# Kernel tuning notes

Measured on AMD Instinct MI355X. Metric: run time of the kernel, lower is better.

The kernel has to match this reference:

```python
import jax, jax.numpy as jnp
import numpy as np

B, DIM, T = 8, 1024, 4096
CB, CD = 4096, 8          # codebook_size, codebook_dim
COMMIT = 0.25
EPS = 1e-12


def _weight_norm(v, g):
    # torch weight_norm over dim=0: per-output-channel norm of v
    n = jnp.sqrt(jnp.sum(v * v, axis=1, keepdims=True))
    return g[:, None] * v / n


def _l2_normalize(x):
    n = jnp.sqrt(jnp.sum(x * x, axis=1, keepdims=True))
    return x / jnp.maximum(n, EPS)


def setup_inputs() -> dict:
    key = jax.random.key(0)
    ks = jax.random.split(key, 5)
    z = jax.random.normal(ks[0], (B, DIM, T), jnp.float32)
    v_in = jax.random.normal(ks[1], (CD, DIM), jnp.float32) * 0.02   # conv1d k=1 weight (squeezed)
    g_in = jnp.sqrt(jnp.sum(v_in * v_in, axis=1))                     # weight_norm init: g = ||v||
    b_in = jnp.zeros((CD,), jnp.float32)
    codebook = jax.random.normal(ks[2], (CB, CD), jnp.float32)        # nn.Embedding default N(0,1)
    v_out = jax.random.normal(ks[3], (DIM, CD), jnp.float32) * 0.02
    g_out = jnp.sqrt(jnp.sum(v_out * v_out, axis=1))
    b_out = jnp.zeros((DIM,), jnp.float32)
    return {"z": z, "v_in": v_in, "g_in": g_in, "b_in": b_in,
            "codebook": codebook, "v_out": v_out, "g_out": g_out, "b_out": b_out}


def reference(z, v_in, g_in, b_in, codebook, v_out, g_out, b_out):
    # in_proj: weight-normed 1x1 Conv1d == per-timestep matmul
    W_in = _weight_norm(v_in, g_in)                              # [CD, DIM]
    z_e = jnp.einsum('od,bdt->bot', W_in, z) + b_in[None, :, None]  # [B, CD, T]

    # decode_latents: normalize encodings and codebook, squared-L2 distances
    enc = z_e.transpose(0, 2, 1).reshape(B * T, CD)              # (b t) d
    e_n = _l2_normalize(enc)                                     # [BT, CD]
    c_n = _l2_normalize(codebook)                                # [CB, CD]
    dist = (jnp.sum(e_n * e_n, axis=1, keepdims=True)
            - 2.0 * (e_n @ c_n.T)
            + jnp.sum(c_n * c_n, axis=1)[None, :])               # [BT, CB]
    indices = jnp.argmin(dist, axis=1).reshape(B, T)             # [B, T] int

    # decode_code: gather UN-normalized codebook, transpose to [B, CD, T]
    z_q = codebook[indices].transpose(0, 2, 1)                   # [B, CD, T]

    # training losses (per-batch), commitment + codebook
    sg = jax.lax.stop_gradient
    commitment_loss = jnp.mean((z_e - sg(z_q)) ** 2, axis=(1, 2)) * COMMIT
    codebook_loss = jnp.mean((z_q - sg(z_e)) ** 2, axis=(1, 2))
    commit_loss = commitment_loss + codebook_loss                # [B]

    # straight-through estimator
    z_q_ste = z_e + sg(z_q - z_e)                                # [B, CD, T]

    # out_proj
    W_out = _weight_norm(v_out, g_out)                           # [DIM, CD]
    out = jnp.einsum('oc,bct->bot', W_out, z_q_ste) + b_out[None, :, None]  # [B, DIM, T]
    return out, indices, commit_loss
```

## Files before the change

kernel.cpp:

```cpp
#include <hip/hip_runtime.h>

#define DIMN 1024
#define TN 4096
#define BN 8
#define CBN 4096
#define CDN 8
#define BTN (BN*TN)
#define OUT_ELEMS (BN*DIMN*TN)

typedef float fx4 __attribute__((ext_vector_type(4)));

#define WS_WINT 0
#define WS_WOUT 8192
#define WS_CN   16384
#define WS_C2   49152
#define WS_LOSS 86016
#define WS_CNT  86024
#define WS_ZEP  360448

#define LH_F    8192
#define LBO_F   8256
#define LZE_F   9296
#define LEN_F   9808
#define LCAND_F 10320
#define LZQ_F   11344
#define LDS_TOT 11856

__device__ __forceinline__ float dot4(float4 a, float4 b) {
    float d = a.x * b.x;
    d = fmaf(a.y, b.y, d);
    d = fmaf(a.z, b.z, d);
    d = fmaf(a.w, b.w, d);
    return d;
}
__device__ __forceinline__ void add4(float4& a, float4 b) {
    a.x += b.x; a.y += b.y; a.z += b.z; a.w += b.w;
}

__global__ __launch_bounds__(256) void k0_prep(
    const float* __restrict__ v_in, const float* __restrict__ g_in,
    const float* __restrict__ codebook, const float* __restrict__ v_out,
    const float* __restrict__ g_out, float* __restrict__ ws) {
    __shared__ float sred[5];
    int blk = blockIdx.x, tid = threadIdx.x;
    if (blk < 8) {
        int o = blk;
        const float* v = v_in + o * DIMN;
        float4 x = *(const float4*)(v + tid * 4);
        float p = x.x * x.x + x.y * x.y + x.z * x.z + x.w * x.w;
        for (int off = 32; off >= 1; off >>= 1) p += __shfl_down(p, off, 64);
        if ((tid & 63) == 0) sred[tid >> 6] = p;
        __syncthreads();
        if (tid == 0) {
            float tot = sred[0] + sred[1] + sred[2] + sred[3];
            sred[4] = g_in[o] / sqrtf(tot);
        }
        __syncthreads();
        float s = sred[4];
        ws[WS_WINT + (tid * 4 + 0) * 8 + o] = x.x * s;
        ws[WS_WINT + (tid * 4 + 1) * 8 + o] = x.y * s;
        ws[WS_WINT + (tid * 4 + 2) * 8 + o] = x.z * s;
        ws[WS_WINT + (tid * 4 + 3) * 8 + o] = x.w * s;
    } else if (blk < 12) {
        int r = (blk - 8) * 256 + tid;
        const float* v = v_out + r * 8;
        float4 a = *(const float4*)v;
        float4 b = *(const float4*)(v + 4);
        float n2 = dot4(a, a) + dot4(b, b);
        float s = g_out[r] / sqrtf(n2);
        *(float4*)(ws + WS_WOUT + r * 8)     = make_float4(a.x*s, a.y*s, a.z*s, a.w*s);
        *(float4*)(ws + WS_WOUT + r * 8 + 4) = make_float4(b.x*s, b.y*s, b.z*s, b.w*s);
    } else if (blk < 28) {
        int j = (blk - 12) * 256 + tid;
        const float* c = codebook + j * 8;
        float4 a = *(const float4*)c;
        float4 b = *(const float4*)(c + 4);
        float n2 = dot4(a, a) + dot4(b, b);
        float inv = 1.0f / fmaxf(sqrtf(n2), 1e-12f);
        float4 na = make_float4(a.x*inv, a.y*inv, a.z*inv, a.w*inv);
        float4 nb = make_float4(b.x*inv, b.y*inv, b.z*inv, b.w*inv);
        *(float4*)(ws + WS_CN + j * 8)     = na;
        *(float4*)(ws + WS_CN + j * 8 + 4) = nb;
        ws[WS_C2 + j] = -0.5f * (dot4(na, na) + dot4(nb, nb));
    } else {
        if (tid < 9) ws[WS_LOSS + tid] = 0.0f;
    }
}

__global__ __launch_bounds__(256) void k1a_ze(
    const float* __restrict__ z, float* __restrict__ ws) {
    __shared__ float wlds[512 * 8];
    int tid = threadIdx.x, blk = blockIdx.x;
    int b = blk >> 5;
    int r = blk & 31;
    int t0 = (r >> 1) * 256;
    int dbase = (r & 1) * 512;
    #pragma unroll
    for (int i = 0; i < 4; i++) {
        int f4 = tid + i * 256;
        *(float4*)(wlds + f4 * 4) = *(const float4*)(ws + WS_WINT + dbase * 8 + f4 * 4);
    }
    __syncthreads();
    int w = tid >> 6, lane = tid & 63;
    const float* zp = z + ((size_t)(b * DIMN + dbase + w * 128)) * TN + t0 + lane * 4;
    float4 acc[8];
    #pragma unroll
    for (int c = 0; c < 8; c++) acc[c] = make_float4(0.f, 0.f, 0.f, 0.f);
    #pragma unroll 8
    for (int dd = 0; dd < 128; ++dd) {
        fx4 zr = __builtin_nontemporal_load((const fx4*)(zp + (size_t)dd * TN));
        const float* wv = wlds + (w * 128 + dd) * 8;
        #pragma unroll
        for (int c = 0; c < 8; c++) {
            float wc = wv[c];
            acc[c].x = fmaf(wc, zr.x, acc[c].x);
            acc[c].y = fmaf(wc, zr.y, acc[c].y);
            acc[c].z = fmaf(wc, zr.z, acc[c].z);
            acc[c].w = fmaf(wc, zr.w, acc[c].w);
        }
    }
    int p = (r & 1) * 4 + w;
    float* op = ws + WS_ZEP + ((size_t)p * BTN + b * TN + t0 + lane * 4) * 8;
    *(float4*)(op +  0) = make_float4(acc[0].x, acc[1].x, acc[2].x, acc[3].x);
    *(float4*)(op +  4) = make_float4(acc[4].x, acc[5].x, acc[6].x, acc[7].x);
    *(float4*)(op +  8) = make_float4(acc[0].y, acc[1].y, acc[2].y, acc[3].y);
    *(float4*)(op + 12) = make_float4(acc[4].y, acc[5].y, acc[6].y, acc[7].y);
    *(float4*)(op + 16) = make_float4(acc[0].z, acc[1].z, acc[2].z, acc[3].z);
    *(float4*)(op + 20) = make_float4(acc[4].z, acc[5].z, acc[6].z, acc[7].z);
    *(float4*)(op + 24) = make_float4(acc[0].w, acc[1].w, acc[2].w, acc[3].w);
    *(float4*)(op + 28) = make_float4(acc[4].w, acc[5].w, acc[6].w, acc[7].w);
}

__global__ __launch_bounds__(256, 2) void k_so(
    const float* __restrict__ b_in, const float* __restrict__ codebook,
    const float* __restrict__ b_out, float* __restrict__ dout,
    float* __restrict__ ws) {
    __shared__ float sp[LDS_TOT];
    int tid = threadIdx.x, blk = blockIdx.x;
    int b = blk >> 6;
    int t0 = (blk & 63) * 64;

    if (tid < 64) {
        int bt = b * TN + t0 + tid;
        float4 za = *(const float4*)(b_in);
        float4 zb = *(const float4*)(b_in + 4);
        #pragma unroll
        for (int p = 0; p < 8; p++) {
            const float* pp = ws + WS_ZEP + ((size_t)p * BTN + bt) * 8;
            add4(za, *(const float4*)(pp));
            add4(zb, *(const float4*)(pp + 4));
        }
        *(float4*)(sp + LZE_F + tid * 8)     = za;
        *(float4*)(sp + LZE_F + tid * 8 + 4) = zb;
        float inv = 1.0f / fmaxf(sqrtf(dot4(za, za) + dot4(zb, zb)), 1e-12f);
        *(float4*)(sp + LEN_F + tid * 8)     = make_float4(za.x*inv, za.y*inv, za.z*inv, za.w*inv);
        *(float4*)(sp + LEN_F + tid * 8 + 4) = make_float4(zb.x*inv, zb.y*inv, zb.z*inv, zb.w*inv);
    } else {
        int i = tid - 64;
        #pragma unroll
        for (int r = 0; r < 12; r++) {
            int f4 = r * 192 + i;
            if (f4 < 2048) {
                *(float4*)(sp + f4 * 4) = *(const float4*)(ws + WS_CN + f4 * 4);
            } else {
                int g = f4 - 2048;
                *(float4*)(sp + LH_F + g * 4) = *(const float4*)(ws + WS_C2 + g * 4);
            }
        }
    }
    __syncthreads();

    int t2 = tid & 31, q = tid >> 5;
    int ta = t2 * 2, tb = ta + 1;
    float ea[8], eb[8];
    {
        float4 a0 = *(const float4*)(sp + LEN_F + ta * 8);
        float4 a1 = *(const float4*)(sp + LEN_F + ta * 8 + 4);
        float4 b0 = *(const float4*)(sp + LEN_F + tb * 8);
        float4 b1 = *(const float4*)(sp + LEN_F + tb * 8 + 4);
        ea[0]=a0.x; ea[1]=a0.y; ea[2]=a0.z; ea[3]=a0.w;
        ea[4]=a1.x; ea[5]=a1.y; ea[6]=a1.z; ea[7]=a1.w;
        eb[0]=b0.x; eb[1]=b0.y; eb[2]=b0.z; eb[3]=b0.w;
        eb[4]=b1.x; eb[5]=b1.y; eb[6]=b1.z; eb[7]=b1.w;
    }

    float bs0 = -3.4e38f, bs1 = -3.4e38f;
    int bj0 = 0, bj1 = 0;
    const float* cbp = sp + q * 128 * 8;
    const float* hp  = sp + LH_F + q * 128;

    for (int c = 0; c < 4; c++) {
        if (c > 0) {
            #pragma unroll
            for (int r = 0; r < 9; r++) {
                int f4 = r * 256 + tid;
                if (f4 < 2048) {
                    *(float4*)(sp + f4 * 4) = *(const float4*)(ws + WS_CN + (size_t)c * 8192 + f4 * 4);
                } else {
                    int g = f4 - 2048;
                    *(float4*)(sp + LH_F + g * 4) = *(const float4*)(ws + WS_C2 + c * 1024 + g * 4);
                }
            }
            __syncthreads();
        }
        int jg = c * 1024 + q * 128;
        #pragma unroll 4
        for (int j = 0; j < 128; ++j) {
            float4 ca = *(const float4*)(cbp + j * 8);
            float4 cc = *(const float4*)(cbp + j * 8 + 4);
            float hh = hp[j];
            float s0 = fmaf(ea[0], ca.x, hh);
            s0 = fmaf(ea[1], ca.y, s0); s0 = fmaf(ea[2], ca.z, s0); s0 = fmaf(ea[3], ca.w, s0);
            s0 = fmaf(ea[4], cc.x, s0); s0 = fmaf(ea[5], cc.y, s0);
            s0 = fmaf(ea[6], cc.z, s0); s0 = fmaf(ea[7], cc.w, s0);
            float s1 = fmaf(eb[0], ca.x, hh);
            s1 = fmaf(eb[1], ca.y, s1); s1 = fmaf(eb[2], ca.z, s1); s1 = fmaf(eb[3], ca.w, s1);
            s1 = fmaf(eb[4], cc.x, s1); s1 = fmaf(eb[5], cc.y, s1);
            s1 = fmaf(eb[6], cc.z, s1); s1 = fmaf(eb[7], cc.w, s1);
            if (s0 > bs0) { bs0 = s0; bj0 = jg + j; }
            if (s1 > bs1) { bs1 = s1; bj1 = jg + j; }
        }
        __syncthreads();
    }

    *(float4*)(sp + LCAND_F + (q * 64 + ta) * 2) =
        make_float4(bs0, __int_as_float(bj0), bs1, __int_as_float(bj1));
    __syncthreads();

    if (tid < 64) {
        int t = tid;
        float2 c0 = *(const float2*)(sp + LCAND_F + t * 2);
        float best = c0.x; int idx = __float_as_int(c0.y);
        #pragma unroll
        for (int q2 = 1; q2 < 8; q2++) {
            float2 cq = *(const float2*)(sp + LCAND_F + (q2 * 64 + t) * 2);
            int j2 = __float_as_int(cq.y);
            if (cq.x > best || (cq.x == best && j2 < idx)) { best = cq.x; idx = j2; }
        }
        dout[(size_t)OUT_ELEMS + b * TN + t0 + t] = (float)idx;
        const float* cq = codebook + (size_t)idx * 8;
        float4 qa = *(const float4*)cq, qb = *(const float4*)(cq + 4);
        sp[LZQ_F + 0*64 + t] = qa.x; sp[LZQ_F + 1*64 + t] = qa.y;
        sp[LZQ_F + 2*64 + t] = qa.z; sp[LZQ_F + 3*64 + t] = qa.w;
        sp[LZQ_F + 4*64 + t] = qb.x; sp[LZQ_F + 5*64 + t] = qb.y;
        sp[LZQ_F + 6*64 + t] = qb.z; sp[LZQ_F + 7*64 + t] = qb.w;
        float4 za = *(const float4*)(sp + LZE_F + t * 8);
        float4 zb = *(const float4*)(sp + LZE_F + t * 8 + 4);
        float4 da = make_float4(za.x-qa.x, za.y-qa.y, za.z-qa.z, za.w-qa.w);
        float4 db = make_float4(zb.x-qb.x, zb.y-qb.y, zb.z-qb.z, zb.w-qb.w);
        float l = dot4(da, da) + dot4(db, db);
        for (int off = 32; off >= 1; off >>= 1) l += __shfl_down(l, off, 64);
        if (t == 0) atomicAdd(ws + WS_LOSS + b, l);
    } else {
        int i = tid - 64;
        #pragma unroll
        for (int r = 0; r < 11; r++) {
            int f4 = r * 192 + i;
            if (f4 < 2048) {
                float4 v = *(const float4*)(ws + WS_WOUT + f4 * 4);
                *(float4*)(sp + f4 * 4 + 4 * (f4 >> 7)) = v;
            }
        }
        #pragma unroll
        for (int r = 0; r < 2; r++) {
            int f = r * 192 + i;
            if (f < 256) {
                float4 v = *(const float4*)(b_out + f * 4);
                int sk = f >> 4;
                sp[LBO_F + f * 4 + sk + 0] = v.x;
                sp[LBO_F + f * 4 + sk + 1] = v.y;
                sp[LBO_F + f * 4 + sk + 2] = v.z;
                sp[LBO_F + f * 4 + sk + 3] = v.w;
            }
        }
    }
    __syncthreads();

    int t4 = tid & 15, og = tid >> 4;
    float4 zr[8];
    #pragma unroll
    for (int c = 0; c < 8; c++) zr[c] = *(const float4*)(sp + LZQ_F + c * 64 + t4 * 4);
    size_t obase = ((size_t)(b * DIMN + og * 64)) * TN + (size_t)(t0 + t4 * 4);
    for (int k = 0; k < 64; k++) {
        int o = og * 64 + k;
        const float* wrow = sp + o * 8 + 4 * og;
        float4 wa = *(const float4*)(wrow);
        float4 wb = *(const float4*)(wrow + 4);
        float bo = sp[LBO_F + o + og];
        float4 acc = make_float4(bo, bo, bo, bo);
        float wc[8] = {wa.x, wa.y, wa.z, wa.w, wb.x, wb.y, wb.z, wb.w};
        #pragma unroll
        for (int c = 0; c < 8; c++) {
            acc.x = fmaf(wc[c], zr[c].x, acc.x);
            acc.y = fmaf(wc[c], zr[c].y, acc.y);
            acc.z = fmaf(wc[c], zr[c].z, acc.z);
            acc.w = fmaf(wc[c], zr[c].w, acc.w);
        }
        acc.x = fminf(fmaxf(acc.x, -8.f), 8.f);
        acc.y = fminf(fmaxf(acc.y, -8.f), 8.f);
        acc.z = fminf(fmaxf(acc.z, -8.f), 8.f);
        acc.w = fminf(fmaxf(acc.w, -8.f), 8.f);
        fx4 st; st.x = acc.x; st.y = acc.y; st.z = acc.z; st.w = acc.w;
        __builtin_nontemporal_store(st, (fx4*)(dout + obase + (size_t)k * TN));
    }

    if (tid == 0) {
        __threadfence();
        unsigned int old = atomicAdd((unsigned int*)(ws + WS_CNT), 1u);
        if (old == 511u) {
            #pragma unroll
            for (int i = 0; i < 8; i++) {
                float v = atomicAdd(ws + WS_LOSS + i, 0.0f);
                dout[(size_t)OUT_ELEMS + BTN + i] = v * (1.25f / 32768.0f);
            }
        }
    }
}

extern "C" void kernel_launch(void* const* d_in, const int* in_sizes, int n_in,
                              void* d_out, int out_size, void* d_ws, size_t ws_size,
                              hipStream_t stream) {
    (void)in_sizes; (void)n_in; (void)out_size; (void)ws_size;
    const float* z        = (const float*)d_in[0];
    const float* v_in     = (const float*)d_in[1];
    const float* g_in     = (const float*)d_in[2];
    const float* b_in     = (const float*)d_in[3];
    const float* codebook = (const float*)d_in[4];
    const float* v_out    = (const float*)d_in[5];
    const float* g_out    = (const float*)d_in[6];
    const float* b_out    = (const float*)d_in[7];
    float* out            = (float*)d_out;
    float* ws             = (float*)d_ws;

    hipLaunchKernelGGL(k0_prep, dim3(29), dim3(256), 0, stream,
                       v_in, g_in, codebook, v_out, g_out, ws);
    hipLaunchKernelGGL(k1a_ze, dim3(256), dim3(256), 0, stream, z, ws);
    hipLaunchKernelGGL(k_so, dim3(512), dim3(256), 0, stream,
                       b_in, codebook, b_out, out, ws);
}
```

Measured before the change: 306.1 us.

## Fuse input projection into search kernel and register-tile codebook argmax

Merges the in-projection kernel into the search/output kernel, so each block computes its own z_e partial sums in LDS instead of writing eight partial planes to global workspace and reading them back. The codebook search is restructured: each thread now holds 8 timesteps in registers and streams codebook entries directly from global/L2 rather than staging 1024-entry chunks in LDS with repeated barriers. Candidates are reduced with cross-lane shuffles. The risks are higher register pressure from the 64-float encoding tile, lower parallelism in the z read (512 blocks, each reading 2-float slices), and codebook reads that now go through cache instead of LDS.

```diff
diff --git a/kernel.cpp b/kernel.cpp
--- a/kernel.cpp
+++ b/kernel.cpp
@@ -9,6 +9,7 @@
 #define OUT_ELEMS (BN*DIMN*TN)
 
 typedef float fx4 __attribute__((ext_vector_type(4)));
+typedef float fx2 __attribute__((ext_vector_type(2)));
 
 #define WS_WINT 0
 #define WS_WOUT 8192
@@ -16,15 +17,14 @@
 #define WS_C2   49152
 #define WS_LOSS 86016
 #define WS_CNT  86024
-#define WS_ZEP  360448
-
-#define LH_F    8192
+
 #define LBO_F   8256
-#define LZE_F   9296
-#define LEN_F   9808
-#define LCAND_F 10320
-#define LZQ_F   11344
-#define LDS_TOT 11856
+#define LZEP_F  9296
+#define LZE_F   13648
+#define LEN_F   14160
+#define LCAND_F 14672
+#define LZQ_F   15184
+#define LDS_TOT 15696
 
 __device__ __forceinline__ float dot4(float4 a, float4 b) {
     float d = a.x * b.x;
@@ -87,144 +87,126 @@
     }
 }
 
-__global__ __launch_bounds__(256) void k1a_ze(
-    const float* __restrict__ z, float* __restrict__ ws) {
-    __shared__ float wlds[512 * 8];
-    int tid = threadIdx.x, blk = blockIdx.x;
-    int b = blk >> 5;
-    int r = blk & 31;
-    int t0 = (r >> 1) * 256;
-    int dbase = (r & 1) * 512;
-    #pragma unroll
-    for (int i = 0; i < 4; i++) {
-        int f4 = tid + i * 256;
-        *(float4*)(wlds + f4 * 4) = *(const float4*)(ws + WS_WINT + dbase * 8 + f4 * 4);
-    }
-    __syncthreads();
-    int w = tid >> 6, lane = tid & 63;
-    const float* zp = z + ((size_t)(b * DIMN + dbase + w * 128)) * TN + t0 + lane * 4;
-    float4 acc[8];
-    #pragma unroll
-    for (int c = 0; c < 8; c++) acc[c] = make_float4(0.f, 0.f, 0.f, 0.f);
-    #pragma unroll 8
-    for (int dd = 0; dd < 128; ++dd) {
-        fx4 zr = __builtin_nontemporal_load((const fx4*)(zp + (size_t)dd * TN));
-        const float* wv = wlds + (w * 128 + dd) * 8;
-        #pragma unroll
-        for (int c = 0; c < 8; c++) {
-            float wc = wv[c];
-            acc[c].x = fmaf(wc, zr.x, acc[c].x);
-            acc[c].y = fmaf(wc, zr.y, acc[c].y);
-            acc[c].z = fmaf(wc, zr.z, acc[c].z);
-            acc[c].w = fmaf(wc, zr.w, acc[c].w);
-        }
-    }
-    int p = (r & 1) * 4 + w;
-    float* op = ws + WS_ZEP + ((size_t)p * BTN + b * TN + t0 + lane * 4) * 8;
-    *(float4*)(op +  0) = make_float4(acc[0].x, acc[1].x, acc[2].x, acc[3].x);
-    *(float4*)(op +  4) = make_float4(acc[4].x, acc[5].x, acc[6].x, acc[7].x);
-    *(float4*)(op +  8) = make_float4(acc[0].y, acc[1].y, acc[2].y, acc[3].y);
-    *(float4*)(op + 12) = make_float4(acc[4].y, acc[5].y, acc[6].y, acc[7].y);
-    *(float4*)(op + 16) = make_float4(acc[0].z, acc[1].z, acc[2].z, acc[3].z);
-    *(float4*)(op + 20) = make_float4(acc[4].z, acc[5].z, acc[6].z, acc[7].z);
-    *(float4*)(op + 24) = make_float4(acc[0].w, acc[1].w, acc[2].w, acc[3].w);
-    *(float4*)(op + 28) = make_float4(acc[4].w, acc[5].w, acc[6].w, acc[7].w);
-}
-
-__global__ __launch_bounds__(256, 2) void k_so(
-    const float* __restrict__ b_in, const float* __restrict__ codebook,
-    const float* __restrict__ b_out, float* __restrict__ dout,
-    float* __restrict__ ws) {
+__global__ __launch_bounds__(256, 2) void k_mega(
+    const float* __restrict__ z, const float* __restrict__ b_in,
+    const float* __restrict__ codebook, const float* __restrict__ b_out,
+    float* __restrict__ dout, float* __restrict__ ws) {
     __shared__ float sp[LDS_TOT];
     int tid = threadIdx.x, blk = blockIdx.x;
     int b = blk >> 6;
     int t0 = (blk & 63) * 64;
 
+    #pragma unroll
+    for (int i = 0; i < 8; i++) {
+        int f4 = tid + i * 256;
+        *(float4*)(sp + f4 * 4) = *(const float4*)(ws + WS_WINT + f4 * 4);
+    }
+    __syncthreads();
+    {
+        int p = tid >> 5, tpair = tid & 31;
+        int tA = tpair * 2;
+        const float* zp = z + ((size_t)(b * DIMN + p * 128)) * TN + t0 + tA;
+        float4 a0a = make_float4(0.f,0.f,0.f,0.f), a0b = make_float4(0.f,0.f,0.f,0.f);
+        float4 a1a = make_float4(0.f,0.f,0.f,0.f), a1b = make_float4(0.f,0.f,0.f,0.f);
+        #pragma unroll 8
+        for (int dd = 0; dd < 128; ++dd) {
+            fx2 zv = __builtin_nontemporal_load((const fx2*)(zp + (size_t)dd * TN));
+            const float* wv = sp + (p * 128 + dd) * 8;
+            float4 w0 = *(const float4*)wv;
+            float4 w1 = *(const float4*)(wv + 4);
+            a0a.x = fmaf(w0.x, zv.x, a0a.x); a0a.y = fmaf(w0.y, zv.x, a0a.y);
+            a0a.z = fmaf(w0.z, zv.x, a0a.z); a0a.w = fmaf(w0.w, zv.x, a0a.w);
+            a0b.x = fmaf(w1.x, zv.x, a0b.x); a0b.y = fmaf(w1.y, zv.x, a0b.y);
+            a0b.z = fmaf(w1.z, zv.x, a0b.z); a0b.w = fmaf(w1.w, zv.x, a0b.w);
+            a1a.x = fmaf(w0.x, zv.y, a1a.x); a1a.y = fmaf(w0.y, zv.y, a1a.y);
+            a1a.z = fmaf(w0.z, zv.y, a1a.z); a1a.w = fmaf(w0.w, zv.y, a1a.w);
+            a1b.x = fmaf(w1.x, zv.y, a1b.x); a1b.y = fmaf(w1.y, zv.y, a1b.y);
+            a1b.z = fmaf(w1.z, zv.y, a1b.z); a1b.w = fmaf(w1.w, zv.y, a1b.w);
+        }
+        float* q0 = sp + LZEP_F + tA * 68 + p * 8;
+        *(float4*)(q0)     = a0a;
+        *(float4*)(q0 + 4) = a0b;
+        float* q1 = sp + LZEP_F + (tA + 1) * 68 + p * 8;
+        *(float4*)(q1)     = a1a;
+        *(float4*)(q1 + 4) = a1b;
+    }
+    __syncthreads();
+
     if (tid < 64) {
-        int bt = b * TN + t0 + tid;
+        int t = tid;
         float4 za = *(const float4*)(b_in);
         float4 zb = *(const float4*)(b_in + 4);
         #pragma unroll
         for (int p = 0; p < 8; p++) {
-            const float* pp = ws + WS_ZEP + ((size_t)p * BTN + bt) * 8;
+            const float* pp = sp + LZEP_F + t * 68 + p * 8;
             add4(za, *(const float4*)(pp));
             add4(zb, *(const float4*)(pp + 4));
         }
-        *(float4*)(sp + LZE_F + tid * 8)     = za;
-        *(float4*)(sp + LZE_F + tid * 8 + 4) = zb;
+        *(float4*)(sp + LZE_F + t * 8)     = za;
+        *(float4*)(sp + LZE_F + t * 8 + 4) = zb;
         float inv = 1.0f / fmaxf(sqrtf(dot4(za, za) + dot4(zb, zb)), 1e-12f);
-        *(float4*)(sp + LEN_F + tid * 8)     = make_float4(za.x*inv, za.y*inv, za.z*inv, za.w*inv);
-        *(float4*)(sp + LEN_F + tid * 8 + 4) = make_float4(zb.x*inv, zb.y*inv, zb.z*inv, zb.w*inv);
-    } else {
-        int i = tid - 64;
-        #pragma unroll
-        for (int r = 0; r < 12; r++) {
-            int f4 = r * 192 + i;
-            if (f4 < 2048) {
-                *(float4*)(sp + f4 * 4) = *(const float4*)(ws + WS_CN + f4 * 4);
-            } else {
-                int g = f4 - 2048;
-                *(float4*)(sp + LH_F + g * 4) = *(const float4*)(ws + WS_C2 + g * 4);
-            }
-        }
-    }
-    __syncthreads();
-
-    int t2 = tid & 31, q = tid >> 5;
-    int ta = t2 * 2, tb = ta + 1;
-    float ea[8], eb[8];
-    {
-        float4 a0 = *(const float4*)(sp + LEN_F + ta * 8);
-        float4 a1 = *(const float4*)(sp + LEN_F + ta * 8 + 4);
-        float4 b0 = *(const float4*)(sp + LEN_F + tb * 8);
-        float4 b1 = *(const float4*)(sp + LEN_F + tb * 8 + 4);
-        ea[0]=a0.x; ea[1]=a0.y; ea[2]=a0.z; ea[3]=a0.w;
-        ea[4]=a1.x; ea[5]=a1.y; ea[6]=a1.z; ea[7]=a1.w;
-        eb[0]=b0.x; eb[1]=b0.y; eb[2]=b0.z; eb[3]=b0.w;
-        eb[4]=b1.x; eb[5]=b1.y; eb[6]=b1.z; eb[7]=b1.w;
-    }
-
-    float bs0 = -3.4e38f, bs1 = -3.4e38f;
-    int bj0 = 0, bj1 = 0;
-    const float* cbp = sp + q * 128 * 8;
-    const float* hp  = sp + LH_F + q * 128;
-
-    for (int c = 0; c < 4; c++) {
-        if (c > 0) {
+        *(float4*)(sp + LEN_F + t * 8)     = make_float4(za.x*inv, za.y*inv, za.z*inv, za.w*inv);
+        *(float4*)(sp + LEN_F + t * 8 + 4) = make_float4(zb.x*inv, zb.y*inv, zb.z*inv, zb.w*inv);
+    }
+    __syncthreads();
+
+    int co = tid >> 3, tt = tid & 7;
+    float en[8][8];
+    #pragma unroll
+    for (int k = 0; k < 8; k++) {
+        float4 u = *(const float4*)(sp + LEN_F + (tt * 8 + k) * 8);
+        float4 v = *(const float4*)(sp + LEN_F + (tt * 8 + k) * 8 + 4);
+        en[k][0]=u.x; en[k][1]=u.y; en[k][2]=u.z; en[k][3]=u.w;
+        en[k][4]=v.x; en[k][5]=v.y; en[k][6]=v.z; en[k][7]=v.w;
+    }
+    float bs[8]; int bj[8];
+    #pragma unroll
+    for (int k = 0; k < 8; k++) { bs[k] = -3.4e38f; bj[k] = 0; }
+    #pragma unroll 1
+    for (int ci = 0; ci < 16; ++ci) {
+        int j0 = ci * 256 + co * 8;
+        #pragma unroll
+        for (int qh = 0; qh < 2; ++qh) {
+            int jq = j0 + qh * 4;
+            const float* cg = ws + WS_CN + (size_t)jq * 8;
+            float4 ca[4], cb[4];
             #pragma unroll
-            for (int r = 0; r < 9; r++) {
-                int f4 = r * 256 + tid;
-                if (f4 < 2048) {
-                    *(float4*)(sp + f4 * 4) = *(const float4*)(ws + WS_CN + (size_t)c * 8192 + f4 * 4);
-                } else {
-                    int g = f4 - 2048;
-                    *(float4*)(sp + LH_F + g * 4) = *(const float4*)(ws + WS_C2 + c * 1024 + g * 4);
+            for (int k = 0; k < 4; k++) {
+                ca[k] = *(const float4*)(cg + k * 8);
+                cb[k] = *(const float4*)(cg + k * 8 + 4);
+            }
+            float4 hqv = *(const float4*)(ws + WS_C2 + jq);
+            float hv[4] = {hqv.x, hqv.y, hqv.z, hqv.w};
+            #pragma unroll
+            for (int k = 0; k < 4; k++) {
+                #pragma unroll
+                for (int t = 0; t < 8; t++) {
+                    float s = fmaf(en[t][0], ca[k].x, hv[k]);
+                    s = fmaf(en[t][1], ca[k].y, s); s = fmaf(en[t][2], ca[k].z, s);
+                    s = fmaf(en[t][3], ca[k].w, s);
+                    s = fmaf(en[t][4], cb[k].x, s); s = fmaf(en[t][5], cb[k].y, s);
+                    s = fmaf(en[t][6], cb[k].z, s); s = fmaf(en[t][7], cb[k].w, s);
+                    if (s > bs[t]) { bs[t] = s; bj[t] = jq + k; }
                 }
             }
-            __syncthreads();
-        }
-        int jg = c * 1024 + q * 128;
-        #pragma unroll 4
-        for (int j = 0; j < 128; ++j) {
-            float4 ca = *(const float4*)(cbp + j * 8);
-            float4 cc = *(const float4*)(cbp + j * 8 + 4);
-            float hh = hp[j];
-            float s0 = fmaf(ea[0], ca.x, hh);
-            s0 = fmaf(ea[1], ca.y, s0); s0 = fmaf(ea[2], ca.z, s0); s0 = fmaf(ea[3], ca.w, s0);
-            s0 = fmaf(ea[4], cc.x, s0); s0 = fmaf(ea[5], cc.y, s0);
-            s0 = fmaf(ea[6], cc.z, s0); s0 = fmaf(ea[7], cc.w, s0);
-            float s1 = fmaf(eb[0], ca.x, hh);
-            s1 = fmaf(eb[1], ca.y, s1); s1 = fmaf(eb[2], ca.z, s1); s1 = fmaf(eb[3], ca.w, s1);
-            s1 = fmaf(eb[4], cc.x, s1); s1 = fmaf(eb[5], cc.y, s1);
-            s1 = fmaf(eb[6], cc.z, s1); s1 = fmaf(eb[7], cc.w, s1);
-            if (s0 > bs0) { bs0 = s0; bj0 = jg + j; }
-            if (s1 > bs1) { bs1 = s1; bj1 = jg + j; }
-        }
-        __syncthreads();
-    }
-
-    *(float4*)(sp + LCAND_F + (q * 64 + ta) * 2) =
-        make_float4(bs0, __int_as_float(bj0), bs1, __int_as_float(bj1));
+        }
+    }
+    #pragma unroll
+    for (int st = 8; st <= 32; st <<= 1) {
+        #pragma unroll
+        for (int t = 0; t < 8; t++) {
+            float os = __shfl_xor(bs[t], st, 64);
+            int   oj = __shfl_xor(bj[t], st, 64);
+            if (os > bs[t] || (os == bs[t] && oj < bj[t])) { bs[t] = os; bj[t] = oj; }
+        }
+    }
+    if ((tid & 63) < 8) {
+        int w = tid >> 6;
+        #pragma unroll
+        for (int k = 0; k < 8; k++)
+            *(float2*)(sp + LCAND_F + (w * 64 + tt * 8 + k) * 2) =
+                make_float2(bs[k], __int_as_float(bj[k]));
+    }
     __syncthreads();
 
     if (tid < 64) {
@@ -232,10 +214,10 @@
         float2 c0 = *(const float2*)(sp + LCAND_F + t * 2);
         float best = c0.x; int idx = __float_as_int(c0.y);
         #pragma unroll
-        for (int q2 = 1; q2 < 8; q2++) {
-            float2 cq = *(const float2*)(sp + LCAND_F + (q2 * 64 + t) * 2);
-            int j2 = __float_as_int(cq.y);
-            if (cq.x > best || (cq.x == best && j2 < idx)) { best = cq.x; idx = j2; }
+        for (int w2 = 1; w2 < 4; w2++) {
+            float2 cw = *(const float2*)(sp + LCAND_F + (w2 * 64 + t) * 2);
+            int j2 = __float_as_int(cw.y);
+            if (cw.x > best || (cw.x == best && j2 < idx)) { best = cw.x; idx = j2; }
         }
         dout[(size_t)OUT_ELEMS + b * TN + t0 + t] = (float)idx;
         const float* cq = codebook + (size_t)idx * 8;
@@ -334,7 +316,6 @@
 
     hipLaunchKernelGGL(k0_prep, dim3(29), dim3(256), 0, stream,
                        v_in, g_in, codebook, v_out, g_out, ws);
-    hipLaunchKernelGGL(k1a_ze, dim3(256), dim3(256), 0, stream, z, ws);
-    hipLaunchKernelGGL(k_so, dim3(512), dim3(256), 0, stream,
-                       b_in, codebook, b_out, out, ws);
-}
+    hipLaunchKernelGGL(k_mega, dim3(512), dim3(256), 0, stream,
+                       z, b_in, codebook, b_out, out, ws);
+}
```

Measured after the change: 294.9 us. 3.7% less time.
